# Kernel optimization log

Measured on AMD Instinct MI355X. Metric: run time of the kernel, lower is better.

The kernel has to match this reference:

```python
import jax, jax.numpy as jnp
import numpy as np

D = 1024      # d_model
H = 16        # nhead
DH = D // H   # head_dim = 64
ROT = DH // 2 # rotary_ndims = 32
FFN = 4096    # d_ffn
B, T, M, N = 4, 1024, 128, 64


def _layernorm(x, g, b, eps=1e-5):
    mu = jnp.mean(x, axis=-1, keepdims=True)
    var = jnp.mean(jnp.square(x - mu), axis=-1, keepdims=True)
    return (x - mu) * jax.lax.rsqrt(var + eps) * g + b


def _rotate_half(x):
    x1, x2 = x[..., : x.shape[-1] // 2], x[..., x.shape[-1] // 2:]
    return jnp.concatenate([-x2, x1], axis=-1)


def setup_inputs() -> dict:
    key = jax.random.key(0)
    ks = jax.random.split(key, 16)
    s = 0.02
    inp = {
        'x': jax.random.normal(ks[0], (B, T, D), jnp.float32),
        'memory': jax.random.normal(ks[1], (B, M, D), jnp.float32),
        'nmr': jax.random.normal(ks[2], (B, N, D), jnp.float32),
        'Wq': jax.random.normal(ks[3], (D, D), jnp.float32) * s,
        'bq': jnp.zeros((D,), jnp.float32),
        'Wk': jax.random.normal(ks[4], (D, D), jnp.float32) * s,
        'bk': jnp.zeros((D,), jnp.float32),
        'Wv': jax.random.normal(ks[5], (D, D), jnp.float32) * s,
        'bv': jnp.zeros((D,), jnp.float32),
        'Wo': jax.random.normal(ks[6], (D, D), jnp.float32) * s,
        'bo': jnp.zeros((D,), jnp.float32),
        'W1': jax.random.normal(ks[7], (D, FFN), jnp.float32) * s,
        'b1': jnp.zeros((FFN,), jnp.float32),
        'W2': jax.random.normal(ks[8], (FFN, D), jnp.float32) * s,
        'b2': jnp.zeros((D,), jnp.float32),
        'ln1_g': jnp.ones((D,), jnp.float32),
        'ln1_b': jnp.zeros((D,), jnp.float32),
        'ln2_g': jnp.ones((D,), jnp.float32),
        'ln2_b': jnp.zeros((D,), jnp.float32),
    }
    return inp


def reference(x, memory, nmr, Wq, bq, Wk, bk, Wv, bv, Wo, bo, W1, b1, W2, b2,
              ln1_g, ln1_b, ln2_g, ln2_b):
    b, t, _ = x.shape
    m, n = memory.shape[1], nmr.shape[1]
    pref = m + n
    L = pref + t

    x_full = jnp.concatenate([memory, nmr, x], axis=1)  # (B, L, D)
    xa = _layernorm(x_full, ln1_g, ln1_b)

    def heads(w, bias):
        return (xa @ w + bias).reshape(b, L, H, DH).transpose(0, 2, 1, 3)  # (B,H,L,DH)

    q = heads(Wq, bq)
    k = heads(Wk, bk)
    v = heads(Wv, bv)

    # partial RoPE on first ROT dims of each head
    pos = jnp.arange(L, dtype=jnp.float32)
    inv_freq = 1.0 / (10000.0 ** (jnp.arange(0, ROT, 2, dtype=jnp.float32) / ROT))
    freqs = pos[:, None] * inv_freq[None, :]              # (L, ROT/2)
    emb = jnp.concatenate([freqs, freqs], axis=-1)        # (L, ROT)
    cos, sin = jnp.cos(emb), jnp.sin(emb)
    qr, qp = q[..., :ROT], q[..., ROT:]
    kr, kp = k[..., :ROT], k[..., ROT:]
    qr = qr * cos + _rotate_half(qr) * sin
    kr = kr * cos + _rotate_half(kr) * sin
    q = jnp.concatenate([qr, qp], axis=-1)
    k = jnp.concatenate([kr, kp], axis=-1)

    # block mask: prefix (memory+nmr) fully bidirectional, target causal,
    # target attends to full prefix, prefix does NOT attend to target.
    i = jnp.arange(L)
    allowed = (i[None, :] < pref) | ((i[:, None] >= pref) & (i[None, :] >= pref)
                                     & (i[None, :] <= i[:, None]))  # (L, L)

    scale = 1.0 / jnp.sqrt(jnp.asarray(DH, jnp.float32))
    scores = jnp.einsum('bhqd,bhkd->bhqk', q, k) * scale
    scores = jnp.where(allowed[None, None], scores, jnp.finfo(scores.dtype).min)
    probs = jax.nn.softmax(scores, axis=-1)
    attn = jnp.einsum('bhqk,bhkd->bhqd', probs, v)        # (B,H,L,DH)
    attn = attn.transpose(0, 2, 1, 3).reshape(b, L, D)

    x_full = attn @ Wo + bo + x_full

    xf = _layernorm(x_full, ln2_g, ln2_b)
    xf = jnp.square(jax.nn.relu(xf @ W1 + b1)) @ W2 + b2
    x_full = x_full + xf

    return x_full[:, pref:]
```

## Files before the change

kernel.cpp:

```cpp
#include <hip/hip_runtime.h>
#include <hip/hip_bf16.h>
#include <math.h>

#define D_   1024
#define H_   16
#define DH_  64
#define FFN_ 4096
#define B_   4
#define T_   1024
#define M_   128
#define N_   64
#define PREF 192
#define L_   1216
#define BL_  (B_*L_)
#define BT_  (B_*T_)

typedef __attribute__((ext_vector_type(4))) float f32x4;
typedef __attribute__((ext_vector_type(8))) short bf16x8;
typedef __attribute__((ext_vector_type(8))) unsigned short u16x8;
typedef const __attribute__((address_space(1))) void gvoid_t;
typedef __attribute__((address_space(3))) void lvoid_t;

#define LGKM0 asm volatile("s_waitcnt lgkmcnt(0)" ::: "memory")
#define CFENCE asm volatile("" ::: "memory")

__device__ __forceinline__ void gl_lds16(const void* g, void* l) {
    __builtin_amdgcn_global_load_lds((gvoid_t*)g, (lvoid_t*)l, 16, 0, 0);
}

__device__ __forceinline__ ushort f2bf(float x) {
    union { __hip_bfloat16 h; ushort u; } cv;
    cv.h = __float2bfloat16(x);
    return cv.u;
}

__device__ __forceinline__ u16x8 pack8(float4 a, float4 b) {
    u16x8 r;
    r[0]=f2bf(a.x); r[1]=f2bf(a.y); r[2]=f2bf(a.z); r[3]=f2bf(a.w);
    r[4]=f2bf(b.x); r[5]=f2bf(b.y); r[6]=f2bf(b.z); r[7]=f2bf(b.w);
    return r;
}

__device__ __forceinline__ float block_reduce_sum256(float v, float* sbuf) {
#pragma unroll
    for (int o = 32; o > 0; o >>= 1) v += __shfl_xor(v, o, 64);
    int w = threadIdx.x >> 6;
    if ((threadIdx.x & 63) == 0) sbuf[w] = v;
    __syncthreads();
    float r = sbuf[0] + sbuf[1] + sbuf[2] + sbuf[3];
    __syncthreads();
    return r;
}

__device__ __forceinline__ void wtr_body(const float* __restrict__ W,
                                         ushort* __restrict__ Wt, int K, int Nc)
{
    __shared__ float tl[64][65];
    int c0 = blockIdx.x << 6, k0 = blockIdx.y << 6;
    int tid = threadIdx.x;
    int rr = tid >> 4, c4 = (tid & 15) << 2;
#pragma unroll
    for (int p = 0; p < 4; ++p) {
        int r = (p << 4) + rr;
        float4 v = *(const float4*)(W + (size_t)(k0 + r) * Nc + c0 + c4);
        tl[r][c4+0] = v.x; tl[r][c4+1] = v.y; tl[r][c4+2] = v.z; tl[r][c4+3] = v.w;
    }
    __syncthreads();
#pragma unroll
    for (int p = 0; p < 4; ++p) {
        int rT = (p << 4) + rr;
        ushort4 uv;
        uv.x = f2bf(tl[c4+0][rT]);
        uv.y = f2bf(tl[c4+1][rT]);
        uv.z = f2bf(tl[c4+2][rT]);
        uv.w = f2bf(tl[c4+3][rT]);
        *(ushort4*)(Wt + (size_t)(c0 + rT) * K + k0 + c4) = uv;
    }
}

__global__ __launch_bounds__(256) void wtr_kernel(
    const float* __restrict__ W, ushort* __restrict__ Wt, int K, int Nc)
{ wtr_body(W, Wt, K, Nc); }

__global__ __launch_bounds__(256) void wtr4_kernel(
    const float* __restrict__ W0, const float* __restrict__ W1,
    const float* __restrict__ W2, const float* __restrict__ W3,
    ushort* __restrict__ T0, ushort* __restrict__ T1,
    ushort* __restrict__ T2, ushort* __restrict__ T3)
{
    const float* W; ushort* T;
    switch (blockIdx.z) {
        case 0: W = W0; T = T0; break;
        case 1: W = W1; T = T1; break;
        case 2: W = W2; T = T2; break;
        default: W = W3; T = T3; break;
    }
    wtr_body(W, T, D_, D_);
}

__global__ __launch_bounds__(256) void prep_kernel(
    float* __restrict__ tab, const float* __restrict__ bq,
    const float* __restrict__ bk, const float* __restrict__ bv,
    float* __restrict__ ob)
{
    int i = blockIdx.x * 256 + threadIdx.x;
    if (i < L_ * 32) {
        int pos = i >> 5, idx = i & 31;
        int fi = idx & 15;
        float invf = exp2f(-(float)fi * 0.83048202372f);
        float th = (float)pos * invf;
        tab[i] = (idx < 16) ? cosf(th) : sinf(th);
    } else {
        int j = i - L_ * 32;
        if (j < 3072) {
            float v = (j < 1024) ? bq[j] : (j < 2048 ? bk[j - 1024] : bv[j - 2048]);
            ob[j] = v;
        }
    }
}

__global__ __launch_bounds__(256) void ln1_concat_kernel(
    const float* __restrict__ x, const float* __restrict__ mem,
    const float* __restrict__ nmr, const float* __restrict__ g,
    const float* __restrict__ be, float* __restrict__ x_full,
    ushort* __restrict__ xa_bf)
{
    __shared__ float sbuf[4];
    int row = blockIdx.x;
    int b = row / L_, pos = row % L_;
    const float* src;
    if (pos < M_)          src = mem + ((size_t)b*M_ + pos)      * D_;
    else if (pos < M_+N_)  src = nmr + ((size_t)b*N_ + (pos-M_)) * D_;
    else                   src = x   + ((size_t)b*T_ + (pos-PREF))*D_;

    int c = threadIdx.x << 2;
    float4 v = *(const float4*)(src + c);
    float s = v.x + v.y + v.z + v.w;
    s = block_reduce_sum256(s, sbuf);
    float mu = s * (1.0f / D_);
    float dx = v.x - mu, dy = v.y - mu, dz = v.z - mu, dw = v.w - mu;
    float q = dx*dx + dy*dy + dz*dz + dw*dw;
    q = block_reduce_sum256(q, sbuf);
    float inv = rsqrtf(q * (1.0f / D_) + 1e-5f);
    float4 gv = *(const float4*)(g + c);
    float4 bv = *(const float4*)(be + c);
    ushort4 o;
    o.x = f2bf(dx*inv*gv.x + bv.x);
    o.y = f2bf(dy*inv*gv.y + bv.y);
    o.z = f2bf(dz*inv*gv.z + bv.z);
    o.w = f2bf(dw*inv*gv.w + bv.w);
    *(float4*)(x_full + (size_t)row*D_ + c) = v;
    *(ushort4*)(xa_bf + (size_t)row*D_ + c) = o;
}

__global__ __launch_bounds__(256) void ln2_kernel(
    const float* __restrict__ src, const float* __restrict__ g,
    const float* __restrict__ be, ushort* __restrict__ dst)
{
    __shared__ float sbuf[4];
    int row = blockIdx.x;
    int c = threadIdx.x << 2;
    float4 v = *(const float4*)(src + (size_t)row*D_ + c);
    float s = v.x + v.y + v.z + v.w;
    s = block_reduce_sum256(s, sbuf);
    float mu = s * (1.0f / D_);
    float dx = v.x - mu, dy = v.y - mu, dz = v.z - mu, dw = v.w - mu;
    float q = dx*dx + dy*dy + dz*dz + dw*dw;
    q = block_reduce_sum256(q, sbuf);
    float inv = rsqrtf(q * (1.0f / D_) + 1e-5f);
    float4 gv = *(const float4*)(g + c);
    float4 bv = *(const float4*)(be + c);
    ushort4 o;
    o.x = f2bf(dx*inv*gv.x + bv.x);
    o.y = f2bf(dy*inv*gv.y + bv.y);
    o.z = f2bf(dz*inv*gv.z + bv.z);
    o.w = f2bf(dw*inv*gv.w + bv.w);
    *(ushort4*)(dst + (size_t)row*D_ + c) = o;
}

__global__ __launch_bounds__(256) void reduce2_out_kernel(
    const float* __restrict__ part, const float* __restrict__ b2,
    const float* __restrict__ x2, float* __restrict__ out)
{
    int row = blockIdx.x;
    int c = threadIdx.x << 2;
    size_t o = (size_t)row * D_ + c;
    const size_t S = (size_t)BT_ * D_;
    float4 p0 = *(const float4*)(part + o);
    float4 p1 = *(const float4*)(part + S + o);
    float4 bb = *(const float4*)(b2 + c);
    float4 rv = *(const float4*)(x2 + o);
    float4 v;
    v.x = p0.x + p1.x + bb.x + rv.x;
    v.y = p0.y + p1.y + bb.y + rv.y;
    v.z = p0.z + p1.z + bb.z + rv.z;
    v.w = p0.w + p1.w + bb.w + rv.w;
    *(float4*)(out + o) = v;
}

template<int MODE, int BW>
__global__ __launch_bounds__(BW*64) void gemmv2_kernel(
    const ushort* __restrict__ A, const ushort* __restrict__ Bt,
    const float* __restrict__ bias, const float* __restrict__ res,
    const float* __restrict__ rtab, void* __restrict__ Cout,
    int Nc, int Kstride, int Klen)
{
    constexpr int BN = BW * 32;
    constexpr int NT = BW * 64;
    constexpr int AP = 1024 / NT;
    __shared__ ushort SM[(49152 + 3*BN*64)/2];
    char* SMb = (char*)SM;

    int tid = threadIdx.x;
    int lane = tid & 63, w = tid >> 6;
    int l15 = lane & 15, l4 = lane >> 4;
    int wm, wn;
    if (BW == 8) { wm = w >> 2; wn = w & 3; }
    else         { wm = w >> 1; wn = w & 1; }

    int nwg = gridDim.x * gridDim.y;
    int flat = blockIdx.y * gridDim.x + blockIdx.x;
    int q = nwg >> 3, r8 = nwg & 7;
    int xcd = flat & 7, idx = flat >> 3;
    int sz = (xcd < r8 ? xcd * (q + 1) : r8 * (q + 1) + (xcd - r8) * q) + idx;
    int row0 = (sz / gridDim.x) * 256, col0 = (sz % gridDim.x) * BN;

    int kbase = blockIdx.z * Klen;

    f32x4 acc[8][4] = {};

    int tr = tid >> 2, sc = tid & 3;
    int lc = sc ^ ((tr >> 1) & 3);
    const ushort* Ag = A  + (size_t)(row0 + tr) * Kstride + kbase + (lc << 3);
    const ushort* Bg = Bt + (size_t)(col0 + tr) * Kstride + kbase + (lc << 3);
    const size_t rstep = (size_t)(NT >> 2) * Kstride;

#define STG(ss, kt)                                                          \
    do { char* Ab = SMb + (ss)*16384; char* Bb = SMb + 49152 + (ss)*(BN*64); \
        size_t ko = (size_t)(kt) << 5;                                       \
        _Pragma("unroll")                                                    \
        for (int p = 0; p < AP; ++p)                                         \
            gl_lds16(Ag + p*rstep + ko, Ab + p*(NT*16) + (tid << 4));        \
        _Pragma("unroll")                                                    \
        for (int p = 0; p < 2; ++p)                                          \
            gl_lds16(Bg + p*rstep + ko, Bb + p*(NT*16) + (tid << 4));        \
    } while (0)

    int nT = Klen >> 5;
    STG(0, 0);
    STG(1, 1);
    int cur = 0;
    for (int t = 0; t < nT; ++t) {
        if (t + 2 < nT) {
            int s2 = cur + 2; if (s2 >= 3) s2 -= 3;
            STG(s2, t + 2);
            if (BW == 8) asm volatile("s_waitcnt vmcnt(8)" ::: "memory");
            else         asm volatile("s_waitcnt vmcnt(12)" ::: "memory");
        } else if (t + 1 < nT) {
            if (BW == 8) asm volatile("s_waitcnt vmcnt(4)" ::: "memory");
            else         asm volatile("s_waitcnt vmcnt(6)" ::: "memory");
        } else {
            asm volatile("s_waitcnt vmcnt(0)" ::: "memory");
        }
        __builtin_amdgcn_s_barrier();
        CFENCE;
        const ushort* As = (const ushort*)(SMb + cur*16384);
        const ushort* Bs = (const ushort*)(SMb + 49152 + cur*(BN*64));
        bf16x8 af[8], bfr[4];
#pragma unroll
        for (int i = 0; i < 8; ++i) {
            int ra = (wm << 7) + (i << 4) + l15;
            af[i] = *(const bf16x8*)(&As[(ra << 5) + ((l4 ^ ((ra >> 1) & 3)) << 3)]);
        }
#pragma unroll
        for (int j = 0; j < 4; ++j) {
            int rb = (wn << 6) + (j << 4) + l15;
            bfr[j] = *(const bf16x8*)(&Bs[(rb << 5) + ((l4 ^ ((rb >> 1) & 3)) << 3)]);
        }
        __builtin_amdgcn_s_setprio(1);
#pragma unroll
        for (int i = 0; i < 8; ++i)
#pragma unroll
            for (int j = 0; j < 4; ++j)
                acc[i][j] = __builtin_amdgcn_mfma_f32_16x16x32_bf16(af[i], bfr[j], acc[i][j], 0, 0, 0);
        __builtin_amdgcn_s_setprio(0);
        CFENCE;
        __builtin_amdgcn_s_barrier();
        cur = (cur + 1 == 3) ? 0 : cur + 1;
    }
#undef STG

    float bcol[4] = {0.f, 0.f, 0.f, 0.f};
    if (MODE != 4) {
#pragma unroll
        for (int j = 0; j < 4; ++j) bcol[j] = bias[col0 + (wn << 6) + (j << 4) + l15];
    }

    float* scr = (float*)SMb + w * 1088;
    int rr = lane >> 2, cseg = lane & 3;
    int colbase = col0 + (wn << 6);
    int hh = ((col0 & 1023) + (wn << 6)) >> 6;
    int which = col0 >> 10;

#pragma unroll
    for (int i = 0; i < 8; ++i) {
        LGKM0;
#pragma unroll
        for (int j = 0; j < 4; ++j)
#pragma unroll
            for (int r = 0; r < 4; ++r) {
                float v = acc[i][j][r] + bcol[j];
                if (MODE == 3) { v = fmaxf(v, 0.f); v *= v; }
                scr[((l4 << 2) + r)*68 + (j << 4) + l15] = v;
            }
        LGKM0;
        int grow = row0 + (wm << 7) + (i << 4) + rr;

        if (MODE == 7 && which == 2) {
            int r0g = row0 + (wm << 7) + (i << 4);
            int bb = r0g / L_;
            int posb = r0g - bb * L_;
            float4 v0, v1, v2, v3;
            v0.x = scr[ 0*68 + lane]; v0.y = scr[ 1*68 + lane];
            v0.z = scr[ 2*68 + lane]; v0.w = scr[ 3*68 + lane];
            v1.x = scr[ 4*68 + lane]; v1.y = scr[ 5*68 + lane];
            v1.z = scr[ 6*68 + lane]; v1.w = scr[ 7*68 + lane];
            v2.x = scr[ 8*68 + lane]; v2.y = scr[ 9*68 + lane];
            v2.z = scr[10*68 + lane]; v2.w = scr[11*68 + lane];
            v3.x = scr[12*68 + lane]; v3.y = scr[13*68 + lane];
            v3.z = scr[14*68 + lane]; v3.w = scr[15*68 + lane];
            ushort* O = (ushort*)Cout + 2*(size_t)BL_*D_;
            size_t base = ((size_t)(bb*H_ + hh)*64 + lane)*L_ + posb;
            *(u16x8*)(O + base)     = pack8(v0, v1);
            *(u16x8*)(O + base + 8) = pack8(v2, v3);
        } else if (MODE == 7) {
            int bb = grow / L_;
            int pos = grow - bb * L_;
            float4 a0 = *(float4*)&scr[rr*68 + (cseg << 4) + 0];
            float4 a1 = *(float4*)&scr[rr*68 + (cseg << 4) + 4];
            float4 a2 = *(float4*)&scr[rr*68 + (cseg << 4) + 8];
            float4 a3 = *(float4*)&scr[rr*68 + (cseg << 4) + 12];
            if (cseg < 2) {
                int oseg = cseg ^ 1;
                float4 p0 = *(float4*)&scr[rr*68 + (oseg << 4) + 0];
                float4 p1 = *(float4*)&scr[rr*68 + (oseg << 4) + 4];
                float4 p2 = *(float4*)&scr[rr*68 + (oseg << 4) + 8];
                float4 p3 = *(float4*)&scr[rr*68 + (oseg << 4) + 12];
                const float* tb = rtab + pos*32;
                float4 c0 = *(const float4*)(tb + 0),  c1 = *(const float4*)(tb + 4);
                float4 c2 = *(const float4*)(tb + 8),  c3 = *(const float4*)(tb + 12);
                float4 s0 = *(const float4*)(tb + 16), s1 = *(const float4*)(tb + 20);
                float4 s2 = *(const float4*)(tb + 24), s3 = *(const float4*)(tb + 28);
                float sg = (cseg == 0) ? -1.f : 1.f;
                a0.x = a0.x*c0.x + sg*p0.x*s0.x; a0.y = a0.y*c0.y + sg*p0.y*s0.y;
                a0.z = a0.z*c0.z + sg*p0.z*s0.z; a0.w = a0.w*c0.w + sg*p0.w*s0.w;
                a1.x = a1.x*c1.x + sg*p1.x*s1.x; a1.y = a1.y*c1.y + sg*p1.y*s1.y;
                a1.z = a1.z*c1.z + sg*p1.z*s1.z; a1.w = a1.w*c1.w + sg*p1.w*s1.w;
                a2.x = a2.x*c2.x + sg*p2.x*s2.x; a2.y = a2.y*c2.y + sg*p2.y*s2.y;
                a2.z = a2.z*c2.z + sg*p2.z*s2.z; a2.w = a2.w*c2.w + sg*p2.w*s2.w;
                a3.x = a3.x*c3.x + sg*p3.x*s3.x; a3.y = a3.y*c3.y + sg*p3.y*s3.y;
                a3.z = a3.z*c3.z + sg*p3.z*s3.z; a3.w = a3.w*c3.w + sg*p3.w*s3.w;
            }
            ushort* O = (ushort*)Cout + (size_t)which * ((size_t)BL_*D_);
            size_t base = (((size_t)(bb*H_ + hh)*L_ + pos) << 6) + (cseg << 4);
            *(u16x8*)(O + base)     = pack8(a0, a1);
            *(u16x8*)(O + base + 8) = pack8(a2, a3);
        } else {
            float4 q0 = *(float4*)&scr[rr*68 + (cseg << 4) + 0];
            float4 q1 = *(float4*)&scr[rr*68 + (cseg << 4) + 4];
            float4 q2 = *(float4*)&scr[rr*68 + (cseg << 4) + 8];
            float4 q3 = *(float4*)&scr[rr*68 + (cseg << 4) + 12];
            int gcol = colbase + (cseg << 4);
            if (MODE == 3) {
                ushort* O = (ushort*)Cout;
                *(u16x8*)(O + (size_t)grow*Nc + gcol)     = pack8(q0, q1);
                *(u16x8*)(O + (size_t)grow*Nc + gcol + 8) = pack8(q2, q3);
            } else if (MODE == 4) {
                float* O = (float*)Cout + (size_t)blockIdx.z * ((size_t)BT_ * D_);
                size_t o = (size_t)grow*Nc + gcol;
                *(float4*)(O + o)      = q0;
                *(float4*)(O + o + 4)  = q1;
                *(float4*)(O + o + 8)  = q2;
                *(float4*)(O + o + 12) = q3;
            } else {
                int rs = (grow >> 10)*L_ + PREF + (grow & (T_-1));
                size_t roff = (size_t)rs*D_ + gcol;
                float4 r0 = *(const float4*)(res + roff);
                float4 r1 = *(const float4*)(res + roff + 4);
                float4 r2 = *(const float4*)(res + roff + 8);
                float4 r3 = *(const float4*)(res + roff + 12);
                q0.x += r0.x; q0.y += r0.y; q0.z += r0.z; q0.w += r0.w;
                q1.x += r1.x; q1.y += r1.y; q1.z += r1.z; q1.w += r1.w;
                q2.x += r2.x; q2.y += r2.y; q2.z += r2.z; q2.w += r2.w;
                q3.x += r3.x; q3.y += r3.y; q3.z += r3.z; q3.w += r3.w;
                float* O = (float*)Cout;
                size_t o = (size_t)grow*Nc + gcol;
                *(float4*)(O + o)      = q0;
                *(float4*)(O + o + 4)  = q1;
                *(float4*)(O + o + 8)  = q2;
                *(float4*)(O + o + 12) = q3;
            }
        }
    }
}

__global__ __launch_bounds__(256) void attn_mfma_kernel(
    const ushort* __restrict__ qhd, const ushort* __restrict__ khd,
    const ushort* __restrict__ vt, ushort* __restrict__ attn_bf)
{
    __shared__ ushort Ks[2][64*64];
    __shared__ ushort Vs[2][64*64];
    __shared__ ushort Ps[4*16*64];

    int bid0 = blockIdx.x;
    int bid = (bid0 & 7) * (gridDim.x >> 3) + (bid0 >> 3);
    int qb = 15 - (bid & 15);
    int h  = (bid >> 4) & (H_ - 1);
    int b  = bid >> 8;
    int tid = threadIdx.x, lane = tid & 63, w = tid >> 6;
    int l15 = lane & 15, lg = lane >> 4;
    int i0 = PREF + (qb << 6);
    int wq0 = w << 4;
    size_t bh = (size_t)(b * H_ + h);

    const ushort* qrow = qhd + (bh * L_ + i0 + wq0 + l15) * 64;
    bf16x8 bq0 = *(const bf16x8*)(qrow + (lg << 3));
    bf16x8 bq1 = *(const bf16x8*)(qrow + 32 + (lg << 3));

    f32x4 acc[4] = {};
    float mrun = -INFINITY;
    float lsum = 0.f;

    int srow = tid >> 3;
    int sslot = tid & 7;
    ushort* Ps_w = Ps + (w << 10);
    const float SC = 0.125f * 1.4426950408889634f;
    int qcap = i0 + wq0 + l15;

#define STAGE_T(buf, t)                                                     \
    do { int j0s = (t) << 6;                                                \
        gl_lds16(khd + (bh * L_ + j0s + srow) * 64 + ((sslot ^ (srow & 7)) << 3),      \
                 (char*)Ks[buf] + (tid << 4));                              \
        gl_lds16(khd + (bh * L_ + j0s + 32 + srow) * 64 + ((sslot ^ ((32+srow) & 7)) << 3), \
                 (char*)Ks[buf] + ((256 + tid) << 4));                      \
        gl_lds16(vt + (bh * 64 + srow) * L_ + j0s + ((sslot ^ (srow & 7)) << 3),       \
                 (char*)Vs[buf] + (tid << 4));                              \
        gl_lds16(vt + (bh * 64 + 32 + srow) * L_ + j0s + ((sslot ^ ((32+srow) & 7)) << 3), \
                 (char*)Vs[buf] + ((256 + tid) << 4));                      \
    } while (0)

    int ntile = 4 + qb;
    STAGE_T(0, 0);
    __syncthreads();
    int cur = 0;
    for (int t = 0; t < ntile; ++t) {
        if (t + 1 < ntile) STAGE_T(cur ^ 1, t + 1);
        const ushort* Kc = Ks[cur];
        const ushort* Vc = Vs[cur];

        f32x4 s4[4];
        __builtin_amdgcn_s_setprio(1);
#pragma unroll
        for (int st = 0; st < 4; ++st) {
            int rk = (st << 4) + l15;
            bf16x8 ak0 = *(const bf16x8*)(Kc + (rk << 6) + ((lg       ^ (rk & 7)) << 3));
            bf16x8 ak1 = *(const bf16x8*)(Kc + (rk << 6) + (((4 + lg) ^ (rk & 7)) << 3));
            f32x4 z = {};
            z = __builtin_amdgcn_mfma_f32_16x16x32_bf16(ak0, bq0, z, 0, 0, 0);
            z = __builtin_amdgcn_mfma_f32_16x16x32_bf16(ak1, bq1, z, 0, 0, 0);
            s4[st] = z;
        }
        __builtin_amdgcn_s_setprio(0);

        int j0 = t << 6;
        float sv[4][4];
        bool diag = (t == ntile - 1);
        int kbq = j0 + (lg << 2);
#pragma unroll
        for (int st = 0; st < 4; ++st)
#pragma unroll
            for (int r = 0; r < 4; ++r) {
                float s = s4[st][r] * SC;
                if (diag && (kbq + (st << 4) + r > qcap)) s = -INFINITY;
                sv[st][r] = s;
            }
        float bm;
        {
            float t0 = fmaxf(fmaxf(sv[0][0], sv[0][1]), fmaxf(sv[0][2], sv[0][3]));
            float t1 = fmaxf(fmaxf(sv[1][0], sv[1][1]), fmaxf(sv[1][2], sv[1][3]));
            float t2 = fmaxf(fmaxf(sv[2][0], sv[2][1]), fmaxf(sv[2][2], sv[2][3]));
            float t3 = fmaxf(fmaxf(sv[3][0], sv[3][1]), fmaxf(sv[3][2], sv[3][3]));
            bm = fmaxf(fmaxf(t0, t1), fmaxf(t2, t3));
        }
        bm = fmaxf(bm, __shfl_xor(bm, 16, 64));
        bm = fmaxf(bm, __shfl_xor(bm, 32, 64));

        float mn = fmaxf(mrun, bm);
        float cr = exp2f(mrun - mn);
        mrun = mn;
        float pe[4][4];
        float ps = 0.f;
#pragma unroll
        for (int st = 0; st < 4; ++st)
#pragma unroll
            for (int r = 0; r < 4; ++r) {
                float e = exp2f(sv[st][r] - mn);
                pe[st][r] = e; ps += e;
            }
        ps += __shfl_xor(ps, 16, 64);
        ps += __shfl_xor(ps, 32, 64);
        lsum = lsum * cr + ps;
#pragma unroll
        for (int su = 0; su < 4; ++su) acc[su] *= cr;

#pragma unroll
        for (int st = 0; st < 4; ++st) {
            int slot = (st << 1) + (lg >> 1);
            int sb = ((lg & 1) << 3);
#pragma unroll
            for (int rp = 0; rp < 2; ++rp) {
                uint u = (uint)f2bf(pe[st][2*rp]) | ((uint)f2bf(pe[st][2*rp+1]) << 16);
                *(uint*)((char*)Ps_w + l15*128 + ((slot ^ (l15 & 7)) << 4) + sb + (rp << 2)) = u;
            }
        }
        {
            bf16x8 bp0 = *(const bf16x8*)((char*)Ps_w + l15*128 + ((lg       ^ (l15 & 7)) << 4));
            bf16x8 bp1 = *(const bf16x8*)((char*)Ps_w + l15*128 + (((4 + lg) ^ (l15 & 7)) << 4));
            __builtin_amdgcn_s_setprio(1);
#pragma unroll
            for (int su = 0; su < 4; ++su) {
                int rd = (su << 4) + l15;
                bf16x8 av0 = *(const bf16x8*)(Vc + (rd << 6) + ((lg       ^ (rd & 7)) << 3));
                bf16x8 av1 = *(const bf16x8*)(Vc + (rd << 6) + (((4 + lg) ^ (rd & 7)) << 3));
                acc[su] = __builtin_amdgcn_mfma_f32_16x16x32_bf16(av0, bp0, acc[su], 0, 0, 0);
                acc[su] = __builtin_amdgcn_mfma_f32_16x16x32_bf16(av1, bp1, acc[su], 0, 0, 0);
            }
            __builtin_amdgcn_s_setprio(0);
        }
        __syncthreads();
        cur ^= 1;
    }
#undef STAGE_T

    float rl = 1.0f / lsum;
    size_t orow = (size_t)b * T_ + (i0 - PREF) + wq0 + l15;
#pragma unroll
    for (int su = 0; su < 4; ++su) {
        ushort4 o4;
        o4.x = f2bf(acc[su][0] * rl);
        o4.y = f2bf(acc[su][1] * rl);
        o4.z = f2bf(acc[su][2] * rl);
        o4.w = f2bf(acc[su][3] * rl);
        *(ushort4*)(attn_bf + orow * D_ + (h << 6) + (su << 4) + (lg << 2)) = o4;
    }
}

extern "C" void kernel_launch(void* const* d_in, const int* in_sizes, int n_in,
                              void* d_out, int out_size, void* d_ws, size_t ws_size,
                              hipStream_t stream) {
    const float* x   = (const float*)d_in[0];
    const float* mem = (const float*)d_in[1];
    const float* nmr = (const float*)d_in[2];
    const float* Wq  = (const float*)d_in[3];
    const float* bq  = (const float*)d_in[4];
    const float* Wk  = (const float*)d_in[5];
    const float* bk  = (const float*)d_in[6];
    const float* Wv  = (const float*)d_in[7];
    const float* bv  = (const float*)d_in[8];
    const float* Wo  = (const float*)d_in[9];
    const float* bo  = (const float*)d_in[10];
    const float* W1  = (const float*)d_in[11];
    const float* b1  = (const float*)d_in[12];
    const float* W2  = (const float*)d_in[13];
    const float* b2  = (const float*)d_in[14];
    const float* g1  = (const float*)d_in[15];
    const float* be1 = (const float*)d_in[16];
    const float* g2  = (const float*)d_in[17];
    const float* be2 = (const float*)d_in[18];
    float* out = (float*)d_out;

    const size_t BLD = (size_t)BL_ * D_;
    const size_t BTD = (size_t)BT_ * D_;

    float* f = (float*)d_ws;
    float* x_full = f;
    float* x2     = f + BLD;
    float* bqkv   = x2 + BTD;
    float* rtab   = bqkv + 4096;
    ushort* bfb   = (ushort*)(rtab + (size_t)L_*32);
    ushort* xa_bf   = bfb;
    ushort* qhd     = bfb + BLD;
    ushort* khd     = bfb + 2*BLD;
    ushort* vt      = bfb + 3*BLD;
    ushort* h1_bf   = bfb + 4*BLD;
    ushort* wq_bf = h1_bf + (size_t)BT_*FFN_;
    ushort* wk_bf = wq_bf + (size_t)D_*D_;
    ushort* wv_bf = wk_bf + (size_t)D_*D_;
    ushort* wo_bf = wv_bf + (size_t)D_*D_;
    ushort* w1_bf = wo_bf + (size_t)D_*D_;
    ushort* w2_bf = w1_bf + (size_t)D_*FFN_;
    float* partials = (float*)(w2_bf + (size_t)FFN_*D_);
    ushort* attn_bf = xa_bf;
    ushort* ln2_bf  = qhd;

    wtr4_kernel<<<dim3(16, 16, 4), 256, 0, stream>>>(Wq, Wk, Wv, Wo,
                                                     wq_bf, wk_bf, wv_bf, wo_bf);
    wtr_kernel<<<dim3(FFN_/64, D_/64),   256, 0, stream>>>(W1, w1_bf, D_,   FFN_);
    wtr_kernel<<<dim3(D_/64,   FFN_/64), 256, 0, stream>>>(W2, w2_bf, FFN_, D_);
    prep_kernel<<<(L_*32 + 3072 + 255)/256, 256, 0, stream>>>(rtab, bq, bk, bv, bqkv);

    ln1_concat_kernel<<<BL_, 256, 0, stream>>>(x, mem, nmr, g1, be1, x_full, xa_bf);

    gemmv2_kernel<7,8><<<dim3(3072/256, BL_/256), 512, 0, stream>>>(
        xa_bf, wq_bf, bqkv, nullptr, rtab, qhd, D_, D_, D_);

    attn_mfma_kernel<<<B_*H_*(T_/64), 256, 0, stream>>>(qhd, khd, vt, attn_bf);

    gemmv2_kernel<2,4><<<dim3(D_/128, BT_/256), 256, 0, stream>>>(
        attn_bf, wo_bf, bo, x_full, nullptr, x2, D_, D_, D_);

    ln2_kernel<<<BT_, 256, 0, stream>>>(x2, g2, be2, ln2_bf);

    gemmv2_kernel<3,8><<<dim3(FFN_/256, BT_/256), 512, 0, stream>>>(
        ln2_bf, w1_bf, b1, nullptr, nullptr, h1_bf, FFN_, D_, D_);

    gemmv2_kernel<4,4><<<dim3(D_/128, BT_/256, 2), 256, 0, stream>>>(
        h1_bf, w2_bf, nullptr, nullptr, nullptr, partials, D_, FFN_, FFN_/2);
    reduce2_out_kernel<<<BT_, 256, 0, stream>>>(partials, b2, x2, out);
}
```

Measured before the change: 254.0 us.

## Add intra-block split-K GEMM for narrow-N projections and fuse residual into LN2

```diff
diff --git a/kernel.cpp b/kernel.cpp
--- a/kernel.cpp
+++ b/kernel.cpp
@@ -153,14 +153,28 @@
     *(ushort4*)(xa_bf + (size_t)row*D_ + c) = o;
 }
 
-__global__ __launch_bounds__(256) void ln2_kernel(
-    const float* __restrict__ src, const float* __restrict__ g,
-    const float* __restrict__ be, ushort* __restrict__ dst)
+__global__ __launch_bounds__(256) void reduce2_ln2_kernel(
+    const float* __restrict__ part, const float* __restrict__ bo,
+    const float* __restrict__ x_full, const float* __restrict__ g,
+    const float* __restrict__ be, float* __restrict__ x2,
+    ushort* __restrict__ ln2_bf)
 {
     __shared__ float sbuf[4];
     int row = blockIdx.x;
     int c = threadIdx.x << 2;
-    float4 v = *(const float4*)(src + (size_t)row*D_ + c);
+    size_t o = (size_t)row * D_ + c;
+    float4 a  = *(const float4*)(part + o);
+    float4 b2 = *(const float4*)(part + (size_t)BT_*D_ + o);
+    float4 bb = *(const float4*)(bo + c);
+    int rr = (row >> 10)*L_ + PREF + (row & (T_-1));
+    float4 rv = *(const float4*)(x_full + (size_t)rr*D_ + c);
+    float4 v;
+    v.x = a.x + b2.x + bb.x + rv.x;
+    v.y = a.y + b2.y + bb.y + rv.y;
+    v.z = a.z + b2.z + bb.z + rv.z;
+    v.w = a.w + b2.w + bb.w + rv.w;
+    *(float4*)(x2 + o) = v;
+
     float s = v.x + v.y + v.z + v.w;
     s = block_reduce_sum256(s, sbuf);
     float mu = s * (1.0f / D_);
@@ -170,12 +184,12 @@
     float inv = rsqrtf(q * (1.0f / D_) + 1e-5f);
     float4 gv = *(const float4*)(g + c);
     float4 bv = *(const float4*)(be + c);
-    ushort4 o;
-    o.x = f2bf(dx*inv*gv.x + bv.x);
-    o.y = f2bf(dy*inv*gv.y + bv.y);
-    o.z = f2bf(dz*inv*gv.z + bv.z);
-    o.w = f2bf(dw*inv*gv.w + bv.w);
-    *(ushort4*)(dst + (size_t)row*D_ + c) = o;
+    ushort4 ov;
+    ov.x = f2bf(dx*inv*gv.x + bv.x);
+    ov.y = f2bf(dy*inv*gv.y + bv.y);
+    ov.z = f2bf(dz*inv*gv.z + bv.z);
+    ov.w = f2bf(dw*inv*gv.w + bv.w);
+    *(ushort4*)(ln2_bf + o) = ov;
 }
 
 __global__ __launch_bounds__(256) void reduce2_out_kernel(
@@ -198,52 +212,184 @@
     *(float4*)(out + o) = v;
 }
 
-template<int MODE, int BW>
-__global__ __launch_bounds__(BW*64) void gemmv2_kernel(
+__global__ __launch_bounds__(512) void gemm_sk8_kernel(
     const ushort* __restrict__ A, const ushort* __restrict__ Bt,
-    const float* __restrict__ bias, const float* __restrict__ res,
-    const float* __restrict__ rtab, void* __restrict__ Cout,
-    int Nc, int Kstride, int Klen)
-{
-    constexpr int BN = BW * 32;
-    constexpr int NT = BW * 64;
-    constexpr int AP = 1024 / NT;
-    __shared__ ushort SM[(49152 + 3*BN*64)/2];
+    float* __restrict__ Cout, int Nc, int Kstride, int Klen)
+{
+    __shared__ ushort SM[73728];
     char* SMb = (char*)SM;
-
     int tid = threadIdx.x;
     int lane = tid & 63, w = tid >> 6;
     int l15 = lane & 15, l4 = lane >> 4;
-    int wm, wn;
-    if (BW == 8) { wm = w >> 2; wn = w & 3; }
-    else         { wm = w >> 1; wn = w & 1; }
+    int g = w >> 2, w4 = w & 3;
+    int wm = w4 >> 1, wn = w4 & 1;
+
+    int nx = gridDim.x;
+    int flat = blockIdx.y * nx + blockIdx.x;
+    int cpx = (nx * gridDim.y) >> 3;
+    int sz = (flat & 7) * cpx + (flat >> 3);
+    int row0 = (sz / nx) * 256, col0 = (sz % nx) * 128;
+
+    f32x4 acc[8][4] = {};
+    const int kl = Klen >> 1;
+    const int kbase = blockIdx.z * Klen + g * kl;
+
+    int gt = tid & 255;
+    int trr = gt >> 2, sc = gt & 3;
+    const ushort* Abase = A  + (size_t)row0 * Kstride + kbase;
+    const ushort* Bbase = Bt + (size_t)col0 * Kstride + kbase;
+    char* AL = SMb + g * 73728;
+    char* BL = AL + 49152;
+
+#define STG(ss, kt)                                                          \
+    do { size_t ko = (size_t)(kt) << 5;                                      \
+        _Pragma("unroll")                                                    \
+        for (int p = 0; p < 4; ++p) {                                        \
+            int rw = (p << 6) + trr; int lc = sc ^ ((rw >> 1) & 3);          \
+            gl_lds16(Abase + (size_t)rw*Kstride + ko + (lc << 3),            \
+                     AL + (ss)*16384 + (p << 12) + (gt << 4));               \
+        }                                                                    \
+        _Pragma("unroll")                                                    \
+        for (int p = 0; p < 2; ++p) {                                        \
+            int rw = (p << 6) + trr; int lc = sc ^ ((rw >> 1) & 3);          \
+            gl_lds16(Bbase + (size_t)rw*Kstride + ko + (lc << 3),            \
+                     BL + (ss)*8192 + (p << 12) + (gt << 4));                \
+        }                                                                    \
+    } while (0)
+
+    int nT = kl >> 5;
+    STG(0, 0);
+    STG(1, 1);
+    int cur = 0;
+    for (int t = 0; t < nT; ++t) {
+        if (t + 2 < nT) {
+            int s2 = cur + 2; if (s2 >= 3) s2 -= 3;
+            STG(s2, t + 2);
+            asm volatile("s_waitcnt vmcnt(12)" ::: "memory");
+        } else if (t + 1 < nT) {
+            asm volatile("s_waitcnt vmcnt(6)" ::: "memory");
+        } else {
+            asm volatile("s_waitcnt vmcnt(0)" ::: "memory");
+        }
+        __builtin_amdgcn_s_barrier();
+        CFENCE;
+        const ushort* As = (const ushort*)(AL + cur*16384);
+        const ushort* Bs = (const ushort*)(BL + cur*8192);
+        bf16x8 af[8], bfr[4];
+#pragma unroll
+        for (int i = 0; i < 8; ++i) {
+            int ra = (wm << 7) + (i << 4) + l15;
+            af[i] = *(const bf16x8*)(&As[(ra << 5) + ((l4 ^ ((ra >> 1) & 3)) << 3)]);
+        }
+#pragma unroll
+        for (int j = 0; j < 4; ++j) {
+            int rb = (wn << 6) + (j << 4) + l15;
+            bfr[j] = *(const bf16x8*)(&Bs[(rb << 5) + ((l4 ^ ((rb >> 1) & 3)) << 3)]);
+        }
+        __builtin_amdgcn_s_setprio(1);
+#pragma unroll
+        for (int i = 0; i < 8; ++i)
+#pragma unroll
+            for (int j = 0; j < 4; ++j)
+                acc[i][j] = __builtin_amdgcn_mfma_f32_16x16x32_bf16(af[i], bfr[j], acc[i][j], 0, 0, 0);
+        __builtin_amdgcn_s_setprio(0);
+        CFENCE;
+        __builtin_amdgcn_s_barrier();
+        cur = (cur + 1 == 3) ? 0 : cur + 1;
+    }
+#undef STG
+
+    float* hs = (float*)SMb;
+#pragma unroll
+    for (int half = 0; half < 2; ++half) {
+        __syncthreads();
+        if (g == 1 && wm == half) {
+#pragma unroll
+            for (int i = 0; i < 8; ++i)
+#pragma unroll
+                for (int j = 0; j < 4; ++j)
+#pragma unroll
+                    for (int r = 0; r < 4; ++r)
+                        hs[((i << 4) + (l4 << 2) + r)*132 + (wn << 6) + (j << 4) + l15] = acc[i][j][r];
+        }
+        __syncthreads();
+        if (g == 0 && wm == half) {
+#pragma unroll
+            for (int i = 0; i < 8; ++i)
+#pragma unroll
+                for (int j = 0; j < 4; ++j)
+#pragma unroll
+                    for (int r = 0; r < 4; ++r)
+                        acc[i][j][r] += hs[((i << 4) + (l4 << 2) + r)*132 + (wn << 6) + (j << 4) + l15];
+        }
+    }
+    __syncthreads();
+    if (g == 1) return;
+
+    float* scr = (float*)SMb + w * 1088;
+    int rr2 = lane >> 2, cseg = lane & 3;
+    float* O = Cout + (size_t)blockIdx.z * ((size_t)BT_ * D_);
+#pragma unroll
+    for (int i = 0; i < 8; ++i) {
+        LGKM0;
+#pragma unroll
+        for (int j = 0; j < 4; ++j)
+#pragma unroll
+            for (int r = 0; r < 4; ++r)
+                scr[((l4 << 2) + r)*68 + (j << 4) + l15] = acc[i][j][r];
+        LGKM0;
+        int grow = row0 + (wm << 7) + (i << 4) + rr2;
+        float4 q0 = *(float4*)&scr[rr2*68 + (cseg << 4) + 0];
+        float4 q1 = *(float4*)&scr[rr2*68 + (cseg << 4) + 4];
+        float4 q2 = *(float4*)&scr[rr2*68 + (cseg << 4) + 8];
+        float4 q3 = *(float4*)&scr[rr2*68 + (cseg << 4) + 12];
+        int gcol = col0 + (wn << 6) + (cseg << 4);
+        size_t o = (size_t)grow*Nc + gcol;
+        *(float4*)(O + o)      = q0;
+        *(float4*)(O + o + 4)  = q1;
+        *(float4*)(O + o + 8)  = q2;
+        *(float4*)(O + o + 12) = q3;
+    }
+}
+
+template<int MODE>
+__global__ __launch_bounds__(512) void gemmv2_kernel(
+    const ushort* __restrict__ A, const ushort* __restrict__ Bt,
+    const float* __restrict__ bias, const float* __restrict__ rtab,
+    void* __restrict__ Cout, int Nc, int Kstride, int Klen)
+{
+    __shared__ ushort SM[(49152 + 49152)/2];
+    char* SMb = (char*)SM;
+
+    int tid = threadIdx.x;
+    int lane = tid & 63, w = tid >> 6;
+    int l15 = lane & 15, l4 = lane >> 4;
+    int wm = w >> 2, wn = w & 3;
 
     int nwg = gridDim.x * gridDim.y;
     int flat = blockIdx.y * gridDim.x + blockIdx.x;
     int q = nwg >> 3, r8 = nwg & 7;
     int xcd = flat & 7, idx = flat >> 3;
     int sz = (xcd < r8 ? xcd * (q + 1) : r8 * (q + 1) + (xcd - r8) * q) + idx;
-    int row0 = (sz / gridDim.x) * 256, col0 = (sz % gridDim.x) * BN;
-
-    int kbase = blockIdx.z * Klen;
+    int row0 = (sz / gridDim.x) * 256, col0 = (sz % gridDim.x) * 256;
 
     f32x4 acc[8][4] = {};
 
     int tr = tid >> 2, sc = tid & 3;
     int lc = sc ^ ((tr >> 1) & 3);
-    const ushort* Ag = A  + (size_t)(row0 + tr) * Kstride + kbase + (lc << 3);
-    const ushort* Bg = Bt + (size_t)(col0 + tr) * Kstride + kbase + (lc << 3);
-    const size_t rstep = (size_t)(NT >> 2) * Kstride;
+    const ushort* Ag = A  + (size_t)(row0 + tr) * Kstride + (lc << 3);
+    const ushort* Bg = Bt + (size_t)(col0 + tr) * Kstride + (lc << 3);
+    const size_t rstep = (size_t)128 * Kstride;
 
 #define STG(ss, kt)                                                          \
-    do { char* Ab = SMb + (ss)*16384; char* Bb = SMb + 49152 + (ss)*(BN*64); \
+    do { char* Ab = SMb + (ss)*16384; char* Bb = SMb + 49152 + (ss)*16384;   \
         size_t ko = (size_t)(kt) << 5;                                       \
         _Pragma("unroll")                                                    \
-        for (int p = 0; p < AP; ++p)                                         \
-            gl_lds16(Ag + p*rstep + ko, Ab + p*(NT*16) + (tid << 4));        \
+        for (int p = 0; p < 2; ++p)                                          \
+            gl_lds16(Ag + p*rstep + ko, Ab + p*8192 + (tid << 4));           \
         _Pragma("unroll")                                                    \
         for (int p = 0; p < 2; ++p)                                          \
-            gl_lds16(Bg + p*rstep + ko, Bb + p*(NT*16) + (tid << 4));        \
+            gl_lds16(Bg + p*rstep + ko, Bb + p*8192 + (tid << 4));           \
     } while (0)
 
     int nT = Klen >> 5;
@@ -254,18 +400,16 @@
         if (t + 2 < nT) {
             int s2 = cur + 2; if (s2 >= 3) s2 -= 3;
             STG(s2, t + 2);
-            if (BW == 8) asm volatile("s_waitcnt vmcnt(8)" ::: "memory");
-            else         asm volatile("s_waitcnt vmcnt(12)" ::: "memory");
+            asm volatile("s_waitcnt vmcnt(8)" ::: "memory");
         } else if (t + 1 < nT) {
-            if (BW == 8) asm volatile("s_waitcnt vmcnt(4)" ::: "memory");
-            else         asm volatile("s_waitcnt vmcnt(6)" ::: "memory");
+            asm volatile("s_waitcnt vmcnt(4)" ::: "memory");
         } else {
             asm volatile("s_waitcnt vmcnt(0)" ::: "memory");
         }
         __builtin_amdgcn_s_barrier();
         CFENCE;
         const ushort* As = (const ushort*)(SMb + cur*16384);
-        const ushort* Bs = (const ushort*)(SMb + 49152 + cur*(BN*64));
+        const ushort* Bs = (const ushort*)(SMb + 49152 + cur*16384);
         bf16x8 af[8], bfr[4];
 #pragma unroll
         for (int i = 0; i < 8; ++i) {
@@ -290,17 +434,15 @@
     }
 #undef STG
 
-    float bcol[4] = {0.f, 0.f, 0.f, 0.f};
-    if (MODE != 4) {
-#pragma unroll
-        for (int j = 0; j < 4; ++j) bcol[j] = bias[col0 + (wn << 6) + (j << 4) + l15];
-    }
+    float bcol[4];
+#pragma unroll
+    for (int j = 0; j < 4; ++j) bcol[j] = bias[col0 + (wn << 6) + (j << 4) + l15];
 
     float* scr = (float*)SMb + w * 1088;
     int rr = lane >> 2, cseg = lane & 3;
     int colbase = col0 + (wn << 6);
     int hh = ((col0 & 1023) + (wn << 6)) >> 6;
-    int which = col0 >> 10;
+    int which = (col0 + (wn << 6)) >> 10;
 
 #pragma unroll
     for (int i = 0; i < 8; ++i) {
@@ -371,35 +513,9 @@
             float4 q2 = *(float4*)&scr[rr*68 + (cseg << 4) + 8];
             float4 q3 = *(float4*)&scr[rr*68 + (cseg << 4) + 12];
             int gcol = colbase + (cseg << 4);
-            if (MODE == 3) {
-                ushort* O = (ushort*)Cout;
-                *(u16x8*)(O + (size_t)grow*Nc + gcol)     = pack8(q0, q1);
-                *(u16x8*)(O + (size_t)grow*Nc + gcol + 8) = pack8(q2, q3);
-            } else if (MODE == 4) {
-                float* O = (float*)Cout + (size_t)blockIdx.z * ((size_t)BT_ * D_);
-                size_t o = (size_t)grow*Nc + gcol;
-                *(float4*)(O + o)      = q0;
-                *(float4*)(O + o + 4)  = q1;
-                *(float4*)(O + o + 8)  = q2;
-                *(float4*)(O + o + 12) = q3;
-            } else {
-                int rs = (grow >> 10)*L_ + PREF + (grow & (T_-1));
-                size_t roff = (size_t)rs*D_ + gcol;
-                float4 r0 = *(const float4*)(res + roff);
-                float4 r1 = *(const float4*)(res + roff + 4);
-                float4 r2 = *(const float4*)(res + roff + 8);
-                float4 r3 = *(const float4*)(res + roff + 12);
-                q0.x += r0.x; q0.y += r0.y; q0.z += r0.z; q0.w += r0.w;
-                q1.x += r1.x; q1.y += r1.y; q1.z += r1.z; q1.w += r1.w;
-                q2.x += r2.x; q2.y += r2.y; q2.z += r2.z; q2.w += r2.w;
-                q3.x += r3.x; q3.y += r3.y; q3.z += r3.z; q3.w += r3.w;
-                float* O = (float*)Cout;
-                size_t o = (size_t)grow*Nc + gcol;
-                *(float4*)(O + o)      = q0;
-                *(float4*)(O + o + 4)  = q1;
-                *(float4*)(O + o + 8)  = q2;
-                *(float4*)(O + o + 12) = q3;
-            }
+            ushort* O = (ushort*)Cout;
+            *(u16x8*)(O + (size_t)grow*Nc + gcol)     = pack8(q0, q1);
+            *(u16x8*)(O + (size_t)grow*Nc + gcol + 8) = pack8(q2, q3);
         }
     }
 }
@@ -611,20 +727,19 @@
 
     ln1_concat_kernel<<<BL_, 256, 0, stream>>>(x, mem, nmr, g1, be1, x_full, xa_bf);
 
-    gemmv2_kernel<7,8><<<dim3(3072/256, BL_/256), 512, 0, stream>>>(
-        xa_bf, wq_bf, bqkv, nullptr, rtab, qhd, D_, D_, D_);
+    gemmv2_kernel<7><<<dim3(3072/256, BL_/256), 512, 0, stream>>>(
+        xa_bf, wq_bf, bqkv, rtab, qhd, D_, D_, D_);
 
     attn_mfma_kernel<<<B_*H_*(T_/64), 256, 0, stream>>>(qhd, khd, vt, attn_bf);
 
-    gemmv2_kernel<2,4><<<dim3(D_/128, BT_/256), 256, 0, stream>>>(
-        attn_bf, wo_bf, bo, x_full, nullptr, x2, D_, D_, D_);
-
-    ln2_kernel<<<BT_, 256, 0, stream>>>(x2, g2, be2, ln2_bf);
-
-    gemmv2_kernel<3,8><<<dim3(FFN_/256, BT_/256), 512, 0, stream>>>(
-        ln2_bf, w1_bf, b1, nullptr, nullptr, h1_bf, FFN_, D_, D_);
-
-    gemmv2_kernel<4,4><<<dim3(D_/128, BT_/256, 2), 256, 0, stream>>>(
-        h1_bf, w2_bf, nullptr, nullptr, nullptr, partials, D_, FFN_, FFN_/2);
+    gemm_sk8_kernel<<<dim3(D_/128, BT_/256, 2), 512, 0, stream>>>(
+        attn_bf, wo_bf, partials, D_, D_, D_/2);
+    reduce2_ln2_kernel<<<BT_, 256, 0, stream>>>(partials, bo, x_full, g2, be2, x2, ln2_bf);
+
+    gemmv2_kernel<3><<<dim3(FFN_/256, BT_/256), 512, 0, stream>>>(
+        ln2_bf, w1_bf, b1, nullptr, h1_bf, FFN_, D_, D_);
+
+    gemm_sk8_kernel<<<dim3(D_/128, BT_/256, 2), 512, 0, stream>>>(
+        h1_bf, w2_bf, partials, D_, FFN_, FFN_/2);
     reduce2_out_kernel<<<BT_, 256, 0, stream>>>(partials, b2, x2, out);
 }
```

Measured after the change: 259.9 us. 2.3% more time.
